# Performance work log

Hardware: AMD Instinct MI355X
Metric: run time of the kernel (lower is better)

The kernel has to match this reference:

```python
import jax, jax.numpy as jnp
import numpy as np

B, N, D = 4096, 32768, 256


def setup_inputs() -> dict:
    key = jax.random.key(0)
    kx, kp = jax.random.split(key)
    x = jax.random.normal(kx, (B, D), dtype=jnp.float32)
    prototypes = jax.random.normal(kp, (N, D), dtype=jnp.float32)
    return {"x": x, "prototypes": prototypes}


def reference(x, prototypes):
    # Brute-force L2 1-NN: faiss IndexFlatL2 exact search, k=1, then gather
    x_sq = jnp.sum(x * x, axis=-1, keepdims=True)            # [B, 1]
    p_sq = jnp.sum(prototypes * prototypes, axis=-1)          # [N]
    dists = x_sq + p_sq[None, :] - 2.0 * (x @ prototypes.T)   # [B, N]
    idx = jnp.argmin(dists, axis=-1)                          # [B]
    return prototypes[idx]                                    # [B, D]
```

## Files before the change

### kernel.cpp

```cpp
#include <hip/hip_runtime.h>
#include <stdint.h>


#define NB 4096
#define NP 32768
#define ND 256
#define NG 512
#define MARGIN 2.0f
#define NSPLIT 8
#define CPB 4096

typedef __attribute__((ext_vector_type(8))) __bf16 bf16x8;
typedef __attribute__((ext_vector_type(4))) __bf16 bf16x4;
typedef __attribute__((ext_vector_type(4))) float f32x4;

static constexpr size_t OFF_PSQ = 0;
static constexpr size_t OFF_XB  = 131072;
static constexpr size_t OFF_PB  = OFF_XB + (size_t)NB * ND * 2;
static constexpr size_t OFF_BM  = OFF_PB + (size_t)NP * ND * 2;
static constexpr size_t WS_NEED = OFF_BM + (size_t)NB * NG * 4;

#define VMCNT(n) asm volatile("s_waitcnt vmcnt(" #n ")" ::: "memory")
#define LGKM(n)  asm volatile("s_waitcnt lgkmcnt(" #n ")" ::: "memory")

__device__ __forceinline__ void gload_lds16(const void* g, void* l) {
    __builtin_amdgcn_global_load_lds(
        (const __attribute__((address_space(1))) uint32_t*)g,
        (__attribute__((address_space(3))) uint32_t*)l, 16, 0, 0);
}
__device__ __forceinline__ unsigned fkey(float f) {
    unsigned u = __float_as_uint(f);
    return (u & 0x80000000u) ? ~u : (u | 0x80000000u);
}
__device__ __forceinline__ float fkey_inv(unsigned u) {
    unsigned o = (u & 0x80000000u) ? (u & 0x7FFFFFFFu) : ~u;
    return __uint_as_float(o);
}
__device__ __forceinline__ unsigned long long umin64(unsigned long long a,
                                                     unsigned long long b) {
    return a < b ? a : b;
}
__device__ __forceinline__ unsigned umin32(unsigned a, unsigned b) {
    return a < b ? a : b;
}

__global__ void prep_kernel(const float* __restrict__ X, const float* __restrict__ P,
                            float* __restrict__ psq, __bf16* __restrict__ Xb,
                            __bf16* __restrict__ Pb) {
    int row  = blockIdx.x * 4 + (threadIdx.x >> 6);
    int lane = threadIdx.x & 63;
    if (row < NP) {
        f32x4 v = ((const f32x4*)(P + (size_t)row * ND))[lane];
        bf16x4 b;
        b.x = (__bf16)v.x; b.y = (__bf16)v.y; b.z = (__bf16)v.z; b.w = (__bf16)v.w;
        ((bf16x4*)(Pb + (size_t)row * ND))[lane] = b;
        float s = v.x*v.x + v.y*v.y + v.z*v.z + v.w*v.w;
        #pragma unroll
        for (int off = 32; off > 0; off >>= 1) s += __shfl_down(s, off);
        if (lane == 0) psq[row] = s;
    } else {
        int r = row - NP;
        f32x4 v = ((const f32x4*)(X + (size_t)r * ND))[lane];
        bf16x4 b;
        b.x = (__bf16)v.x; b.y = (__bf16)v.y; b.z = (__bf16)v.z; b.w = (__bf16)v.w;
        ((bf16x4*)(Xb + (size_t)r * ND))[lane] = b;
    }
}

__global__ __launch_bounds__(512, 2)
void nn_pw_kernel(const __bf16* __restrict__ Xb, const __bf16* __restrict__ Pb,
                  const float* __restrict__ psq,
                  unsigned* __restrict__ blockmin) {
    __shared__ __align__(16) char smem[163840];
    char* A_lds = smem;
    char* rings = smem + 65536;

    const int tid  = threadIdx.x;
    const int lane = tid & 63;
    const int wave = tid >> 6;
    const int wm = wave >> 2, wn = wave & 3;
    const int bid    = blockIdx.x;
    const int nsplit = bid & 7;
    const int mblk   = bid >> 3;
    const int bm     = mblk * 128;
    const int Nb     = nsplit * CPB;
    const int fr = lane & 15, kg = lane >> 4;
    const int wbase16 = (tid & ~63) * 16;
    char* ringw = rings + (size_t)wave * 12288;

    f32x4 acc[4][4];
    #pragma unroll
    for (int i = 0; i < 4; ++i)
        #pragma unroll
        for (int j = 0; j < 4; ++j) acc[i][j] = (f32x4){0.f, 0.f, 0.f, 0.f};

    auto stage = [&](int p) {
        char* dst = ringw + (size_t)(p % 3) * 4096;
        const int colb = Nb + (p >> 3) * 256 + wn * 64;
        const int kq   = p & 7;
        #pragma unroll
        for (int i = 0; i < 4; ++i)
            gload_lds16(Pb + (size_t)(colb + i * 16 + fr) * ND + kq * 32 + kg * 8,
                        dst + i * 1024);
    };

    #pragma unroll
    for (int i = 0; i < 8; ++i) {
        const int c  = i * 512 + tid;
        const int q  = c >> 9;
        const int fm = (c >> 6) & 7;
        const int l  = c & 63;
        gload_lds16(Xb + (size_t)(bm + fm * 16 + (l & 15)) * ND +
                        q * 32 + (l >> 4) * 8,
                    A_lds + (size_t)(i * 512) * 16 + wbase16);
    }
    stage(0); stage(1); stage(2);
    VMCNT(8);
    __builtin_amdgcn_s_barrier();
    __builtin_amdgcn_sched_barrier(0);

    bf16x8 av[2][4], bv[2][4];
    #pragma unroll
    for (int mi = 0; mi < 4; ++mi)
        av[0][mi] = *(const bf16x8*)(A_lds +
            (size_t)(((0 * 8) + wm * 4 + mi) * 64 + lane) * 16);
    #pragma unroll
    for (int ni = 0; ni < 4; ++ni)
        bv[0][ni] = *(const bf16x8*)(ringw + (size_t)(ni * 1024 + lane * 16));

    #pragma unroll 1
    for (int nt = 0; nt < 16; ++nt) {
        #pragma unroll
        for (int q = 0; q < 8; ++q) {
            const int t   = nt * 8 + q;
            const int cur = q & 1, nxt = cur ^ 1;
            if (t < 126) { VMCNT(4); }
            else         { VMCNT(0); }
            __builtin_amdgcn_sched_barrier(0);
            if (t < 127) {
                const int qn = (q + 1) & 7;
                #pragma unroll
                for (int mi = 0; mi < 4; ++mi)
                    av[nxt][mi] = *(const bf16x8*)(A_lds +
                        (size_t)((qn * 8 + wm * 4 + mi) * 64 + lane) * 16);
                const char* pc = ringw + (size_t)((t + 1) % 3) * 4096;
                #pragma unroll
                for (int ni = 0; ni < 4; ++ni)
                    bv[nxt][ni] = *(const bf16x8*)(pc +
                        (size_t)(ni * 1024 + lane * 16));
            }
            LGKM(8);
            if (t <= 124) stage(t + 3);
            __builtin_amdgcn_s_setprio(1);
            #pragma unroll
            for (int mi = 0; mi < 4; ++mi)
                #pragma unroll
                for (int ni = 0; ni < 4; ++ni)
                    acc[mi][ni] = __builtin_amdgcn_mfma_f32_16x16x32_bf16(
                        av[cur][mi], bv[cur][ni], acc[mi][ni], 0, 0, 0);
            __builtin_amdgcn_s_setprio(0);

            if (q == 7) {
                const int colb = Nb + nt * 256 + wn * 64;
                float cq[4];
                #pragma unroll
                for (int ni = 0; ni < 4; ++ni)
                    cq[ni] = psq[colb + ni * 16 + fr];
                const int g = nsplit * 64 + nt * 4 + wn;
                #pragma unroll
                for (int mi = 0; mi < 4; ++mi) {
                    #pragma unroll
                    for (int r = 0; r < 4; ++r) {
                        float d = fmaf(-2.f, acc[mi][0][r], cq[0]);
                        #pragma unroll
                        for (int ni = 1; ni < 4; ++ni)
                            d = fminf(d, fmaf(-2.f, acc[mi][ni][r], cq[ni]));
                        #pragma unroll
                        for (int m = 1; m < 16; m <<= 1)
                            d = fminf(d, __shfl_xor(d, m));
                        if (fr == 0)
                            blockmin[(size_t)(bm + wm * 64 + mi * 16 + kg * 4
                                              + r) * NG + g] = fkey(d);
                    }
                }
                #pragma unroll
                for (int i = 0; i < 4; ++i)
                    #pragma unroll
                    for (int j = 0; j < 4; ++j)
                        acc[i][j] = (f32x4){0.f, 0.f, 0.f, 0.f};
            }
        }
    }
}

__global__ __launch_bounds__(512, 2)
void rescore_wave_kernel(const float* __restrict__ X, const float* __restrict__ P,
                         const float* __restrict__ psq,
                         const unsigned* __restrict__ blockmin,
                         float* __restrict__ out) {
    __shared__ float Xs[8][256];
    __shared__ unsigned short wcand[8][512];
    __shared__ int wcnt[8];

    const int tid = threadIdx.x, lane = tid & 63, wv = tid >> 6;
    const int row = blockIdx.x * 8 + wv;

    ((f32x4*)Xs[wv])[lane] = ((const f32x4*)(X + (size_t)row * ND))[lane];
    if (lane == 0) wcnt[wv] = 0;

    const unsigned* bmr = blockmin + (size_t)row * NG;
    uint4 ka = ((const uint4*)bmr)[lane * 2];
    uint4 kb = ((const uint4*)bmr)[lane * 2 + 1];
    unsigned km = umin32(umin32(umin32(ka.x, ka.y), umin32(ka.z, ka.w)),
                         umin32(umin32(kb.x, kb.y), umin32(kb.z, kb.w)));
    #pragma unroll
    for (int m = 1; m < 64; m <<= 1) km = umin32(km, __shfl_xor(km, m));
    const unsigned thr = fkey(fkey_inv(km) + MARGIN);

    const unsigned k8[8] = {ka.x, ka.y, ka.z, ka.w, kb.x, kb.y, kb.z, kb.w};
    #pragma unroll
    for (int i = 0; i < 8; ++i)
        if (k8[i] <= thr)
            wcand[wv][atomicAdd(&wcnt[wv], 1)] = (unsigned short)(lane * 8 + i);
    LGKM(0);
    const int n = wcnt[wv];

    unsigned long long best = 0xFFFFFFFFFFFFFFFFull;
    const f32x4* x4 = (const f32x4*)Xs[wv];
    for (int c = 0; c < n; ++c) {
        const int col = (int)wcand[wv][c] * 64 + lane;
        const f32x4* p4 = (const f32x4*)(P + (size_t)col * ND);
        float s = 0.f;
        #pragma unroll 16
        for (int i = 0; i < 64; ++i) {
            f32x4 pv = p4[i], xv = x4[i];
            s = fmaf(xv.x, pv.x, s); s = fmaf(xv.y, pv.y, s);
            s = fmaf(xv.z, pv.z, s); s = fmaf(xv.w, pv.w, s);
        }
        float d = fmaf(-2.f, s, psq[col]);
        best = umin64(best, ((unsigned long long)fkey(d) << 32) |
                            (unsigned long long)(unsigned)col);
    }
    #pragma unroll
    for (int m = 1; m < 64; m <<= 1)
        best = umin64(best, __shfl_xor(best, m));
    const unsigned bc = (unsigned)(best & 0xFFFFFFFFull);
    ((f32x4*)(out + (size_t)row * ND))[lane] =
        ((const f32x4*)(P + (size_t)bc * ND))[lane];
}

#define BM1 128
#define BN1 128
#define BK1 32
#define LDA1 132

__global__ void psq_init_kernel(const float* __restrict__ P, float* __restrict__ psq,
                                unsigned long long* __restrict__ minpack) {
    int row  = blockIdx.x * 4 + (threadIdx.x >> 6);
    int lane = threadIdx.x & 63;
    float4 p4 = ((const float4*)(P + (size_t)row * ND))[lane];
    float s = p4.x*p4.x + p4.y*p4.y + p4.z*p4.z + p4.w*p4.w;
    #pragma unroll
    for (int off = 32; off > 0; off >>= 1) s += __shfl_down(s, off);
    if (lane == 0) psq[row] = s;
    int gid = blockIdx.x * blockDim.x + threadIdx.x;
    if (gid < NB) minpack[gid] = 0xFFFFFFFFFFFFFFFFull;
}

__global__ __launch_bounds__(256, 2)
void nn_main_kernel(const float* __restrict__ X, const float* __restrict__ P,
                    const float* __restrict__ psq,
                    unsigned long long* __restrict__ minpack) {
    __shared__ __align__(16) char smem_raw[2 * BK1 * LDA1 * 4];
    float (*As)[LDA1] = (float (*)[LDA1])smem_raw;
    float (*Bs)[LDA1] = (float (*)[LDA1])(smem_raw + BK1 * LDA1 * 4);
    const int bm  = blockIdx.y * BM1;
    const int bn  = blockIdx.x * BN1;
    const int tid = threadIdx.x;
    const int tx  = tid & 15;
    const int ty  = tid >> 4;
    float acc[8][8];
    #pragma unroll
    for (int i = 0; i < 8; ++i)
        #pragma unroll
        for (int j = 0; j < 8; ++j) acc[i][j] = 0.f;
    const int lrow = tid >> 3;
    const int lk   = (tid & 7) * 4;
    for (int k0 = 0; k0 < ND; k0 += BK1) {
        #pragma unroll
        for (int p = 0; p < 4; ++p) {
            int r = p * 32 + lrow;
            float4 aa = *(const float4*)(X + (size_t)(bm + r) * ND + k0 + lk);
            As[lk+0][r] = aa.x; As[lk+1][r] = aa.y; As[lk+2][r] = aa.z; As[lk+3][r] = aa.w;
            float4 bb = *(const float4*)(P + (size_t)(bn + r) * ND + k0 + lk);
            Bs[lk+0][r] = bb.x; Bs[lk+1][r] = bb.y; Bs[lk+2][r] = bb.z; Bs[lk+3][r] = bb.w;
        }
        __syncthreads();
        #pragma unroll 4
        for (int k = 0; k < BK1; ++k) {
            float4 a0 = *(const float4*)&As[k][ty*8];
            float4 a1 = *(const float4*)&As[k][ty*8 + 4];
            float4 b0 = *(const float4*)&Bs[k][tx*4];
            float4 b1 = *(const float4*)&Bs[k][64 + tx*4];
            float av2[8] = {a0.x,a0.y,a0.z,a0.w,a1.x,a1.y,a1.z,a1.w};
            float bv2[8] = {b0.x,b0.y,b0.z,b0.w,b1.x,b1.y,b1.z,b1.w};
            #pragma unroll
            for (int i = 0; i < 8; ++i)
                #pragma unroll
                for (int j = 0; j < 8; ++j)
                    acc[i][j] = fmaf(av2[i], bv2[j], acc[i][j]);
        }
        __syncthreads();
    }
    unsigned long long (*red)[16] = (unsigned long long (*)[16])smem_raw;
    float cj[8];
    int   jglob[8];
    #pragma unroll
    for (int j = 0; j < 8; ++j) {
        int c = (j < 4) ? (tx*4 + j) : (64 + tx*4 + (j - 4));
        jglob[j] = bn + c;
        cj[j]    = psq[bn + c];
    }
    #pragma unroll
    for (int i = 0; i < 8; ++i) {
        float bestv = 0.f; unsigned bidx = 0u; bool first = true;
        #pragma unroll
        for (int j = 0; j < 8; ++j) {
            float s = fmaf(-2.f, acc[i][j], cj[j]);
            if (first || s < bestv) { bestv = s; bidx = (unsigned)jglob[j]; first = false; }
        }
        unsigned u = fkey(bestv);
        red[ty*8 + i][tx] = ((unsigned long long)u << 32) | (unsigned long long)bidx;
    }
    __syncthreads();
    if (tid < BM1) {
        unsigned long long m = red[tid][0];
        #pragma unroll
        for (int t = 1; t < 16; ++t) m = umin64(m, red[tid][t]);
        atomicMin(&minpack[bm + tid], m);
    }
}

__global__ void gather_kernel(const float* __restrict__ P,
                              const unsigned long long* __restrict__ minpack,
                              float* __restrict__ out) {
    int row = blockIdx.x;
    unsigned idx = (unsigned)(minpack[row] & 0xFFFFFFFFull);
    int lane = threadIdx.x;
    ((float4*)(out + (size_t)row * ND))[lane] =
        ((const float4*)(P + (size_t)idx * ND))[lane];
}

extern "C" void kernel_launch(void* const* d_in, const int* in_sizes, int n_in,
                              void* d_out, int out_size, void* d_ws, size_t ws_size,
                              hipStream_t stream) {
    const float* X = (const float*)d_in[0];
    const float* P = (const float*)d_in[1];
    float* out = (float*)d_out;
    char* w = (char*)d_ws;

    if (ws_size >= WS_NEED) {
        float* psq = (float*)(w + OFF_PSQ);
        __bf16* Xb = (__bf16*)(w + OFF_XB);
        __bf16* Pb = (__bf16*)(w + OFF_PB);
        unsigned* blockmin = (unsigned*)(w + OFF_BM);

        prep_kernel<<<(NP + NB) / 4, 256, 0, stream>>>(X, P, psq, Xb, Pb);
        nn_pw_kernel<<<(NB / 128) * NSPLIT, 512, 0, stream>>>(Xb, Pb, psq,
                                                              blockmin);
        rescore_wave_kernel<<<NB / 8, 512, 0, stream>>>(X, P, psq, blockmin, out);
    } else {
        float* psq = (float*)w;
        unsigned long long* minpack = (unsigned long long*)(w + (size_t)NP * 4);
        psq_init_kernel<<<NP / 4, 256, 0, stream>>>(P, psq, minpack);
        dim3 grid(NP / BN1, NB / BM1);
        nn_main_kernel<<<grid, dim3(256), 0, stream>>>(X, P, psq, minpack);
        gather_kernel<<<NB, 64, 0, stream>>>(P, minpack, out);
    }
}
```

Before: 212.1 us.

## Share B tile ring across waves, use DPP min reduction, stage blockmin in LDS

Replaces the per-wave private prototype rings with a block-shared 4-deep ring that all waves load cooperatively, so each wave now issues fewer global-to-LDS loads per k-step. This needs a block barrier every step. The 16-lane min reduction switches from shfl_xor to DPP row operations. Per-group minima are written to an LDS table and flushed to global memory at the end with coalesced 8-byte stores, and the psq loads are hoisted to the start of each tile. The per-step barriers add synchronisation cost, which may offset the gains from fewer loads, cheaper shuffles and coalesced stores.

```diff
diff --git a/kernel.cpp b/kernel.cpp
--- a/kernel.cpp
+++ b/kernel.cpp
@@ -27,6 +27,18 @@
     __builtin_amdgcn_global_load_lds(
         (const __attribute__((address_space(1))) uint32_t*)g,
         (__attribute__((address_space(3))) uint32_t*)l, 16, 0, 0);
+}
+__device__ __forceinline__ float dppmin16(float v) {
+    int x;
+    x = __builtin_amdgcn_update_dpp(0, __float_as_int(v), 0xB1, 0xF, 0xF, true);
+    v = fminf(v, __int_as_float(x));
+    x = __builtin_amdgcn_update_dpp(0, __float_as_int(v), 0x4E, 0xF, 0xF, true);
+    v = fminf(v, __int_as_float(x));
+    x = __builtin_amdgcn_update_dpp(0, __float_as_int(v), 0x141, 0xF, 0xF, true);
+    v = fminf(v, __int_as_float(x));
+    x = __builtin_amdgcn_update_dpp(0, __float_as_int(v), 0x140, 0xF, 0xF, true);
+    v = fminf(v, __int_as_float(x));
+    return v;
 }
 __device__ __forceinline__ unsigned fkey(float f) {
     unsigned u = __float_as_uint(f);
@@ -68,12 +80,13 @@
 }
 
 __global__ __launch_bounds__(512, 2)
-void nn_pw_kernel(const __bf16* __restrict__ Xb, const __bf16* __restrict__ Pb,
-                  const float* __restrict__ psq,
-                  unsigned* __restrict__ blockmin) {
+void nn_dpp_kernel(const __bf16* __restrict__ Xb, const __bf16* __restrict__ Pb,
+                   const float* __restrict__ psq,
+                   unsigned* __restrict__ blockmin) {
     __shared__ __align__(16) char smem[163840];
-    char* A_lds = smem;
-    char* rings = smem + 65536;
+    char* ring  = smem;
+    char* A_lds = smem + 65536;
+    unsigned (*tbl)[64] = (unsigned (*)[64])(smem + 131072);
 
     const int tid  = threadIdx.x;
     const int lane = tid & 63;
@@ -86,7 +99,6 @@
     const int Nb     = nsplit * CPB;
     const int fr = lane & 15, kg = lane >> 4;
     const int wbase16 = (tid & ~63) * 16;
-    char* ringw = rings + (size_t)wave * 12288;
 
     f32x4 acc[4][4];
     #pragma unroll
@@ -95,13 +107,18 @@
         for (int j = 0; j < 4; ++j) acc[i][j] = (f32x4){0.f, 0.f, 0.f, 0.f};
 
     auto stage = [&](int p) {
-        char* dst = ringw + (size_t)(p % 3) * 4096;
-        const int colb = Nb + (p >> 3) * 256 + wn * 64;
+        char* dst = ring + (size_t)(p & 3) * 16384;
+        const int colb = Nb + (p >> 3) * 256;
         const int kq   = p & 7;
         #pragma unroll
-        for (int i = 0; i < 4; ++i)
-            gload_lds16(Pb + (size_t)(colb + i * 16 + fr) * ND + kq * 32 + kg * 8,
-                        dst + i * 1024);
+        for (int i = 0; i < 2; ++i) {
+            const int c = i * 512 + tid;
+            const int fn = c >> 6;
+            const int l  = c & 63;
+            gload_lds16(Pb + (size_t)(colb + fn * 16 + (l & 15)) * ND +
+                            kq * 32 + (l >> 4) * 8,
+                        dst + i * 8192 + wbase16);
+        }
     };
 
     #pragma unroll
@@ -115,7 +132,7 @@
                     A_lds + (size_t)(i * 512) * 16 + wbase16);
     }
     stage(0); stage(1); stage(2);
-    VMCNT(8);
+    VMCNT(4);
     __builtin_amdgcn_s_barrier();
     __builtin_amdgcn_sched_barrier(0);
 
@@ -123,19 +140,23 @@
     #pragma unroll
     for (int mi = 0; mi < 4; ++mi)
         av[0][mi] = *(const bf16x8*)(A_lds +
-            (size_t)(((0 * 8) + wm * 4 + mi) * 64 + lane) * 16);
+            (size_t)((wm * 4 + mi) * 64 + lane) * 16);
     #pragma unroll
     for (int ni = 0; ni < 4; ++ni)
-        bv[0][ni] = *(const bf16x8*)(ringw + (size_t)(ni * 1024 + lane * 16));
+        bv[0][ni] = *(const bf16x8*)(ring +
+            (size_t)((wn * 4 + ni) * 64 + lane) * 16);
 
     #pragma unroll 1
     for (int nt = 0; nt < 16; ++nt) {
+        float cq[4];
         #pragma unroll
         for (int q = 0; q < 8; ++q) {
-            const int t   = nt * 8 + q;
+            const int t = nt * 8 + q;
             const int cur = q & 1, nxt = cur ^ 1;
-            if (t < 126) { VMCNT(4); }
-            else         { VMCNT(0); }
+            if (t >= 126)            { VMCNT(0); }
+            else if (q == 1 || q == 2) { VMCNT(6); }
+            else                     { VMCNT(2); }
+            __builtin_amdgcn_s_barrier();
             __builtin_amdgcn_sched_barrier(0);
             if (t < 127) {
                 const int qn = (q + 1) & 7;
@@ -143,14 +164,19 @@
                 for (int mi = 0; mi < 4; ++mi)
                     av[nxt][mi] = *(const bf16x8*)(A_lds +
                         (size_t)((qn * 8 + wm * 4 + mi) * 64 + lane) * 16);
-                const char* pc = ringw + (size_t)((t + 1) % 3) * 4096;
+                const char* pc = ring + (size_t)((t + 1) & 3) * 16384;
                 #pragma unroll
                 for (int ni = 0; ni < 4; ++ni)
                     bv[nxt][ni] = *(const bf16x8*)(pc +
-                        (size_t)(ni * 1024 + lane * 16));
+                        (size_t)((wn * 4 + ni) * 64 + lane) * 16);
             }
-            LGKM(8);
             if (t <= 124) stage(t + 3);
+            if (q == 0) {
+                const int colb = Nb + nt * 256 + wn * 64;
+                #pragma unroll
+                for (int ni = 0; ni < 4; ++ni)
+                    cq[ni] = psq[colb + ni * 16 + fr];
+            }
             __builtin_amdgcn_s_setprio(1);
             #pragma unroll
             for (int mi = 0; mi < 4; ++mi)
@@ -161,12 +187,7 @@
             __builtin_amdgcn_s_setprio(0);
 
             if (q == 7) {
-                const int colb = Nb + nt * 256 + wn * 64;
-                float cq[4];
-                #pragma unroll
-                for (int ni = 0; ni < 4; ++ni)
-                    cq[ni] = psq[colb + ni * 16 + fr];
-                const int g = nsplit * 64 + nt * 4 + wn;
+                const int g = nt * 4 + wn;
                 #pragma unroll
                 for (int mi = 0; mi < 4; ++mi) {
                     #pragma unroll
@@ -175,12 +196,9 @@
                         #pragma unroll
                         for (int ni = 1; ni < 4; ++ni)
                             d = fminf(d, fmaf(-2.f, acc[mi][ni][r], cq[ni]));
-                        #pragma unroll
-                        for (int m = 1; m < 16; m <<= 1)
-                            d = fminf(d, __shfl_xor(d, m));
+                        d = dppmin16(d);
                         if (fr == 0)
-                            blockmin[(size_t)(bm + wm * 64 + mi * 16 + kg * 4
-                                              + r) * NG + g] = fkey(d);
+                            tbl[wm * 64 + mi * 16 + kg * 4 + r][g] = fkey(d);
                     }
                 }
                 #pragma unroll
@@ -190,6 +208,16 @@
                         acc[i][j] = (f32x4){0.f, 0.f, 0.f, 0.f};
             }
         }
+    }
+
+    __syncthreads();
+    #pragma unroll
+    for (int i = 0; i < 8; ++i) {
+        const int f2  = i * 512 + tid;
+        uint2 v = ((const uint2*)tbl)[f2];
+        const int idx = f2 * 2;
+        const int row = idx >> 6, col = idx & 63;
+        *(uint2*)&blockmin[(size_t)(bm + row) * NG + nsplit * 64 + col] = v;
     }
 }
 
@@ -366,8 +394,8 @@
         unsigned* blockmin = (unsigned*)(w + OFF_BM);
 
         prep_kernel<<<(NP + NB) / 4, 256, 0, stream>>>(X, P, psq, Xb, Pb);
-        nn_pw_kernel<<<(NB / 128) * NSPLIT, 512, 0, stream>>>(Xb, Pb, psq,
-                                                              blockmin);
+        nn_dpp_kernel<<<(NB / 128) * NSPLIT, 512, 0, stream>>>(Xb, Pb, psq,
+                                                               blockmin);
         rescore_wave_kernel<<<NB / 8, 512, 0, stream>>>(X, P, psq, blockmin, out);
     } else {
         float* psq = (float*)w;
```

Result: faster. 170.1 us (median of 3 runs) (-19.8%).
